# Optimization experiments

Measured on AMD Instinct MI355X. Metric: run time of the kernel, lower is better.

## Reference

```python
import jax, jax.numpy as jnp
import numpy as np

N = 50000      # nodes
E = 400000     # edges (before self-loops)
IN = 128       # in_channels
OUT = 64       # out_channels (per-head; concat=False averages heads)
HEADS = 8      # heads of first GAT layer; second layer has 1 head
NEG_SLOPE = 0.2


def _glorot(key, shape, fan_in, fan_out):
    s = jnp.sqrt(2.0 / (fan_in + fan_out)).astype(jnp.float32)
    return jax.random.normal(key, shape, jnp.float32) * s


def setup_inputs() -> dict:
    key = jax.random.key(0)
    ks = jax.random.split(key, 10)
    x = jax.random.normal(ks[0], (N, IN), jnp.float32)
    edge_index = jax.random.randint(ks[1], (2, E), 0, N)
    # layer 1: heads=HEADS, per-head dim OUT
    W1 = _glorot(ks[2], (IN, HEADS * OUT), IN, HEADS * OUT)
    att_src1 = _glorot(ks[3], (HEADS, OUT), OUT, 1)
    att_dst1 = _glorot(ks[4], (HEADS, OUT), OUT, 1)
    b1 = jnp.zeros((OUT,), jnp.float32)
    # layer 2: heads=1
    W2 = _glorot(ks[5], (OUT, 1 * OUT), OUT, OUT)
    att_src2 = _glorot(ks[6], (1, OUT), OUT, 1)
    att_dst2 = _glorot(ks[7], (1, OUT), OUT, 1)
    b2 = jnp.zeros((OUT,), jnp.float32)
    return dict(x=x, edge_index=edge_index, W1=W1, att_src1=att_src1,
                att_dst1=att_dst1, b1=b1, W2=W2, att_src2=att_src2,
                att_dst2=att_dst2, b2=b2)


def gat_conv(x, edge_index, W, att_src, att_dst, bias, heads, ch):
    """PyG GATConv with concat=False (mean over heads), add_self_loops=True."""
    n = x.shape[0]
    loop = jnp.arange(n, dtype=edge_index.dtype)
    src = jnp.concatenate([edge_index[0], loop])  # [E+N]
    dst = jnp.concatenate([edge_index[1], loop])
    h = (x @ W).reshape(n, heads, ch)                     # [N, H, C]
    a_s = jnp.sum(h * att_src, axis=-1)                   # [N, H]
    a_d = jnp.sum(h * att_dst, axis=-1)                   # [N, H]
    e = jax.nn.leaky_relu(a_s[src] + a_d[dst], NEG_SLOPE)  # [E+N, H]
    # numerically stable segment softmax over incoming edges of each dst node
    emax = jax.lax.stop_gradient(
        jax.ops.segment_max(e, dst, num_segments=n))       # [N, H]
    ee = jnp.exp(e - emax[dst])
    denom = jax.ops.segment_sum(ee, dst, num_segments=n)  # [N, H]
    alpha = ee / denom[dst]                                # [E+N, H]
    out = jax.ops.segment_sum(alpha[:, :, None] * h[src], dst,
                              num_segments=n)              # [N, H, C]
    return out.mean(axis=1) + bias                         # [N, C]


def reference(x, edge_index, W1, att_src1, att_dst1, b1,
              W2, att_src2, att_dst2, b2):
    h = gat_conv(x, edge_index, W1, att_src1, att_dst1, b1, HEADS, OUT)
    h = jax.nn.elu(h)
    return gat_conv(h, edge_index, W2, att_src2, att_dst2, b2, 1, OUT)
```

## Files before the change

kernel.cpp:

```cpp
#include <hip/hip_runtime.h>
#include <cstdint>
#include <cstddef>

#define NEG_SLOPE 0.2f

typedef short bf16x8 __attribute__((ext_vector_type(8)));
typedef float f32x4 __attribute__((ext_vector_type(4)));
typedef float f32x2 __attribute__((ext_vector_type(2)));

__device__ __forceinline__ unsigned short f2bf(float f) {
  unsigned u = __float_as_uint(f);
  u = u + 0x7FFFu + ((u >> 16) & 1u);
  return (unsigned short)(u >> 16);
}
__device__ __forceinline__ float bf2f(unsigned short b) {
  return __uint_as_float((unsigned)b << 16);
}
__device__ __forceinline__ f32x2 unpk(unsigned xv) {
  f32x2 r;
  r.x = __uint_as_float(xv << 16);
  r.y = __uint_as_float(xv & 0xFFFF0000u);
  return r;
}

__global__ __launch_bounds__(256) void prep_all(
    const int* __restrict__ ei, int* __restrict__ counts,
    const float* __restrict__ x, unsigned short* __restrict__ xb,
    const float* __restrict__ W1, const float* __restrict__ att_s1,
    const float* __restrict__ att_d1, unsigned short* __restrict__ AsAdT,
    unsigned short* __restrict__ WbT,
    const float* __restrict__ W2, unsigned short* __restrict__ W2t,
    const float* __restrict__ att_s2, const float* __restrict__ att_d2,
    float* __restrict__ AsAd2,
    int E, int ET, int N, int B0, int B1) {
  int b = blockIdx.x, tid = threadIdx.x;
  if (b < B0) {
    int i = b * 256 + tid;
    if (i < ET) {
      int dst = (i < E) ? ei[E + i] : (i - E);
      atomicAdd(&counts[dst], 1);
    }
    return;
  }
  b -= B0;
  if (b < B1) {
    int i = b * 256 + tid;
    if (i < N * 32) {
      float4 v = ((const float4*)x)[i];
      ushort4 o;
      o.x = f2bf(v.x); o.y = f2bf(v.y); o.z = f2bf(v.z); o.w = f2bf(v.w);
      ((ushort4*)xb)[i] = o;
    }
    return;
  }
  b -= B1;
  if (b < 8) {
    int i = b * 256 + tid;
    int o = i >> 7, k = i & 127, h = o & 7;
    const float* att = (o < 8) ? att_s1 : att_d1;
    float s = 0.f;
    for (int c = 0; c < 64; c++) s += W1[(size_t)k * 512 + h * 64 + c] * att[h * 64 + c];
    AsAdT[i] = f2bf(s);
    return;
  }
  b -= 8;
  if (b < 256) {
    int i = b * 256 + tid;
    int o = i >> 10, k = i & 1023, h = k >> 7, c = k & 127;
    WbT[i] = f2bf(W1[(size_t)c * 512 + h * 64 + o]);
    return;
  }
  b -= 256;
  if (b < 16) {
    int i = b * 256 + tid;
    if (i < 64 * 64) {
      int k = i >> 6, nn = i & 63;
      W2t[(size_t)nn * 64 + k] = f2bf(W2[i]);
    }
    return;
  }
  {
    int i = tid;
    if (i < 128) {
      int o = i >> 6, k = i & 63;
      const float* att = (o == 0) ? att_s2 : att_d2;
      float s = 0.f;
      for (int c = 0; c < 64; c++) s += W2[(size_t)k * 64 + c] * att[c];
      AsAd2[i] = s;
    }
  }
}

__global__ __launch_bounds__(1024) void scan_dots(
    const int* __restrict__ counts, int* __restrict__ offsets,
    const unsigned short* __restrict__ xb, const unsigned short* __restrict__ AsAdT,
    float* __restrict__ asd, int n) {
  if (blockIdx.x == 0) {
    __shared__ int sums[1024];
    int t = threadIdx.x;
    int chunk = (n + 1023) >> 10;
    int start = t * chunk;
    int end = min(start + chunk, n);
    int s = 0;
    for (int i = start; i < end; i++) s += counts[i];
    sums[t] = s;
    __syncthreads();
    for (int off = 1; off < 1024; off <<= 1) {
      int v = (t >= off) ? sums[t - off] : 0;
      __syncthreads();
      sums[t] += v;
      __syncthreads();
    }
    int run = sums[t] - s;
    for (int i = start; i < end; i++) { offsets[i] = run; run += counts[i]; }
    if (t == 1023) offsets[n] = sums[1023];
    return;
  }
  int tid = threadIdx.x;
  int wave = tid >> 6, lane = tid & 63;
  int q = lane >> 4, t = lane & 15;
  int row0 = (blockIdx.x - 1) * 256 + wave * 16;
  int arow = row0 + t; if (arow > n - 1) arow = n - 1;
  const bf16x8* aptr = (const bf16x8*)(xb + (size_t)arow * 128);
  const bf16x8* bptr = (const bf16x8*)(AsAdT + t * 128);
  f32x4 acc = (f32x4){0.f, 0.f, 0.f, 0.f};
  #pragma unroll
  for (int s = 0; s < 4; s++)
    acc = __builtin_amdgcn_mfma_f32_16x16x32_bf16(aptr[s * 4 + q], bptr[s * 4 + q],
                                                  acc, 0, 0, 0);
  #pragma unroll
  for (int r = 0; r < 4; r++) {
    int row = row0 + q * 4 + r;
    if (row < n) asd[row * 16 + t] = acc[r];
  }
}

__global__ __launch_bounds__(256) void fill_weights(
    const int* __restrict__ ei, const int* __restrict__ offsets,
    int* __restrict__ cursor, int* __restrict__ srcs,
    const float* __restrict__ asd, float* __restrict__ wbuf,
    int E, int ET) {
  int i = blockIdx.x * 256 + threadIdx.x;
  if (i >= ET) return;
  int src, dst;
  if (i < E) { src = ei[i]; dst = ei[E + i]; } else { src = dst = i - E; }
  int pos = atomicAdd(&cursor[dst], 1);
  int slot = offsets[dst] + pos;
  srcs[slot] = src;
  float4 s0 = *(const float4*)&asd[src * 16];
  float4 s1 = *(const float4*)&asd[src * 16 + 4];
  float4 d0 = *(const float4*)&asd[dst * 16 + 8];
  float4 d1 = *(const float4*)&asd[dst * 16 + 12];
  float w[8];
  w[0] = s0.x + d0.x; w[1] = s0.y + d0.y; w[2] = s0.z + d0.z; w[3] = s0.w + d0.w;
  w[4] = s1.x + d1.x; w[5] = s1.y + d1.y; w[6] = s1.z + d1.z; w[7] = s1.w + d1.w;
  #pragma unroll
  for (int h = 0; h < 8; h++) {
    float v = w[h];
    v = (v > 0.f) ? v : NEG_SLOPE * v;
    w[h] = __expf(v);
  }
  float4* wp = (float4*)&wbuf[(size_t)slot * 8];
  wp[0] = make_float4(w[0], w[1], w[2], w[3]);
  wp[1] = make_float4(w[4], w[5], w[6], w[7]);
}

__global__ __launch_bounds__(1024, 8) void agg1_gemm(
    const int* __restrict__ offsets, const int* __restrict__ srcs,
    const float* __restrict__ wbuf, const unsigned short* __restrict__ xb,
    const unsigned short* __restrict__ WbT, const float* __restrict__ b1,
    const float* __restrict__ AsAd2, unsigned short* __restrict__ zb,
    float* __restrict__ as2, float* __restrict__ ad2, int N) {
  __shared__ unsigned short sh[16 * 1032];
  __shared__ int ssrc[16][64];
  __shared__ float sas[16], sad[16];
  int tid = threadIdx.x;
  int wv = tid >> 6, lane = tid & 63;
  int nb = blockIdx.x;
  {
    int row = wv;
    int node = nb * 16 + row;
    float2 acc[8];
    float ws[8];
    #pragma unroll
    for (int h = 0; h < 8; h++) { acc[h].x = 0.f; acc[h].y = 0.f; ws[h] = 0.f; }
    int beg = offsets[node], end = offsets[node + 1];
    for (int cb = beg; cb < end; cb += 64) {
      int cnt = min(64, end - cb);
      if (lane < cnt) ssrc[row][lane] = srcs[cb + lane];
      #pragma unroll 4
      for (int k = 0; k < cnt; k++) {
        int s = ssrc[row][k];
        unsigned xv = *(const unsigned*)&xb[(size_t)s * 128 + 2 * lane];
        float4 wa = *(const float4*)&wbuf[(size_t)(cb + k) * 8];
        float4 wb = *(const float4*)&wbuf[(size_t)(cb + k) * 8 + 4];
        float x0 = __uint_as_float(xv << 16);
        float x1 = __uint_as_float(xv & 0xFFFF0000u);
        acc[0].x += wa.x * x0; acc[0].y += wa.x * x1; ws[0] += wa.x;
        acc[1].x += wa.y * x0; acc[1].y += wa.y * x1; ws[1] += wa.y;
        acc[2].x += wa.z * x0; acc[2].y += wa.z * x1; ws[2] += wa.z;
        acc[3].x += wa.w * x0; acc[3].y += wa.w * x1; ws[3] += wa.w;
        acc[4].x += wb.x * x0; acc[4].y += wb.x * x1; ws[4] += wb.x;
        acc[5].x += wb.y * x0; acc[5].y += wb.y * x1; ws[5] += wb.y;
        acc[6].x += wb.z * x0; acc[6].y += wb.z * x1; ws[6] += wb.z;
        acc[7].x += wb.w * x0; acc[7].y += wb.w * x1; ws[7] += wb.w;
      }
    }
    #pragma unroll
    for (int h = 0; h < 8; h++) {
      float iv = 0.125f / ws[h];
      unsigned o = (unsigned)f2bf(acc[h].x * iv) | ((unsigned)f2bf(acc[h].y * iv) << 16);
      *(unsigned*)&sh[row * 1032 + h * 128 + 2 * lane] = o;
    }
  }
  if (tid < 16) sas[tid] = 0.f;
  else if (tid < 32) sad[tid - 16] = 0.f;
  __syncthreads();
  if (wv < 4) {
    int q = lane >> 4, t = lane & 15;
    f32x4 acc4 = (f32x4){0.f, 0.f, 0.f, 0.f};
    const unsigned short* bbase = WbT + (size_t)(wv * 16 + t) * 1024;
    #pragma unroll 8
    for (int s = 0; s < 32; s++) {
      bf16x8 af = *(const bf16x8*)&sh[t * 1032 + s * 32 + q * 8];
      bf16x8 bf = *(const bf16x8*)&bbase[s * 32 + q * 8];
      acc4 = __builtin_amdgcn_mfma_f32_16x16x32_bf16(af, bf, acc4, 0, 0, 0);
    }
    int col = wv * 16 + t;
    float bias = b1[col];
    float vs = AsAd2[col], vd = AsAd2[64 + col];
    float zr[4];
    #pragma unroll
    for (int r = 0; r < 4; r++) {
      int row = q * 4 + r;
      int node = nb * 16 + row;
      float v = acc4[r] + bias;
      v = (v > 0.f) ? v : (__expf(v) - 1.f);
      zr[r] = v;
      zb[(size_t)node * 64 + col] = f2bf(v);
    }
    #pragma unroll
    for (int r = 0; r < 4; r++) {
      float s = zr[r] * vs, d = zr[r] * vd;
      #pragma unroll
      for (int off = 1; off < 16; off <<= 1) {
        s += __shfl_xor(s, off, 64);
        d += __shfl_xor(d, off, 64);
      }
      if (t == 0) {
        atomicAdd(&sas[q * 4 + r], s);
        atomicAdd(&sad[q * 4 + r], d);
      }
    }
  }
  __syncthreads();
  if (tid < 16) as2[nb * 16 + tid] = sas[tid];
  else if (tid < 32) ad2[nb * 16 + (tid - 16)] = sad[tid - 16];
}

__global__ __launch_bounds__(1024, 8) void agg2_gemm(
    const int* __restrict__ offsets, const int* __restrict__ srcs,
    const float* __restrict__ as2, const float* __restrict__ ad2,
    const unsigned short* __restrict__ zb, const unsigned short* __restrict__ W2t,
    const float* __restrict__ b2, float* __restrict__ out, int N) {
  __shared__ unsigned short sh[16 * 72];
  __shared__ int ssrc[16][64];
  int tid = threadIdx.x;
  int wv = tid >> 6, lane = tid & 63;
  int nb = blockIdx.x;
  {
    int row = wv;
    int node = nb * 16 + row;
    int half = lane >> 5;
    int l2 = lane & 31;
    float adv = ad2[node];
    int beg = offsets[node], end = offsets[node + 1];
    f32x2 acc = (f32x2){0.f, 0.f};
    float ws = 0.f;
    for (int cb = beg; cb < end; cb += 64) {
      int cnt = min(64, end - cb);
      if (lane < cnt) ssrc[row][lane] = srcs[cb + lane];
      #pragma unroll 2
      for (int k = half; k < cnt; k += 2) {
        int s = ssrc[row][k];
        float asv = as2[s];
        unsigned zv = *(const unsigned*)&zb[(size_t)s * 64 + 2 * l2];
        float v = asv + adv;
        v = (v > 0.f) ? v : NEG_SLOPE * v;
        float w = __expf(v);
        ws += w;
        acc += unpk(zv) * w;
      }
    }
    acc.x += __shfl_xor(acc.x, 32, 64);
    acc.y += __shfl_xor(acc.y, 32, 64);
    ws += __shfl_xor(ws, 32, 64);
    if (half == 0) {
      float inv = 1.f / ws;
      unsigned o = (unsigned)f2bf(acc.x * inv) | ((unsigned)f2bf(acc.y * inv) << 16);
      *(unsigned*)&sh[row * 72 + 2 * l2] = o;
    }
  }
  __syncthreads();
  if (wv < 4) {
    int q = lane >> 4, t = lane & 15;
    f32x4 acc4 = (f32x4){0.f, 0.f, 0.f, 0.f};
    const unsigned short* bbase = W2t + (size_t)(wv * 16 + t) * 64;
    #pragma unroll
    for (int s = 0; s < 2; s++) {
      bf16x8 af = *(const bf16x8*)&sh[t * 72 + s * 32 + q * 8];
      bf16x8 bf = *(const bf16x8*)&bbase[s * 32 + q * 8];
      acc4 = __builtin_amdgcn_mfma_f32_16x16x32_bf16(af, bf, acc4, 0, 0, 0);
    }
    int col = wv * 16 + t;
    float bias = b2[col];
    #pragma unroll
    for (int r = 0; r < 4; r++) {
      int node = nb * 16 + q * 4 + r;
      if (node < N) out[(size_t)node * 64 + col] = acc4[r] + bias;
    }
  }
}

extern "C" void kernel_launch(void* const* d_in, const int* in_sizes, int n_in,
                              void* d_out, int out_size, void* d_ws, size_t ws_size,
                              hipStream_t stream) {
  const int IN = 128;
  const int N = in_sizes[0] / IN;
  const int E = in_sizes[1] / 2;
  const int ET = E + N;

  const float* x        = (const float*)d_in[0];
  const int*   ei       = (const int*)d_in[1];
  const float* W1       = (const float*)d_in[2];
  const float* att_src1 = (const float*)d_in[3];
  const float* att_dst1 = (const float*)d_in[4];
  const float* b1       = (const float*)d_in[5];
  const float* W2       = (const float*)d_in[6];
  const float* att_src2 = (const float*)d_in[7];
  const float* att_dst2 = (const float*)d_in[8];
  const float* b2       = (const float*)d_in[9];
  float* out = (float*)d_out;

  char* base = (char*)d_ws;
  size_t off = 0;
  auto alloc = [&](size_t bytes) -> char* {
    char* p = base + off;
    off = (off + bytes + 255) & ~(size_t)255;
    return p;
  };
  unsigned short* xb    = (unsigned short*)alloc((size_t)N * 128 * 2);
  unsigned short* AsAdT = (unsigned short*)alloc((size_t)16 * 128 * 2);
  unsigned short* WbT   = (unsigned short*)alloc((size_t)64 * 1024 * 2);
  unsigned short* W2t   = (unsigned short*)alloc((size_t)64 * 64 * 2);
  unsigned short* zb    = (unsigned short*)alloc((size_t)N * 64 * 2);
  float* AsAd2 = (float*)alloc((size_t)128 * 4);
  float* asd1  = (float*)alloc((size_t)N * 16 * 4);
  float* a_s2  = (float*)alloc((size_t)N * 4);
  float* a_d2  = (float*)alloc((size_t)N * 4);
  float* wbuf  = (float*)alloc((size_t)ET * 8 * 4);
  int* offsets = (int*)alloc((size_t)(N + 1) * 4);
  int* srcs    = (int*)alloc((size_t)ET * 4);
  char* zero_begin = base + off;
  int* counts  = (int*)alloc((size_t)N * 4);
  int* cursor  = (int*)alloc((size_t)N * 4);
  char* zero_end = base + off;

  hipMemsetAsync(zero_begin, 0, (size_t)(zero_end - zero_begin), stream);

  const int TB = 256;
  auto cdiv = [](int a, int b) { return (a + b - 1) / b; };

  int B0 = cdiv(ET, TB);
  int B1 = cdiv(N * 32, TB);
  prep_all<<<B0 + B1 + 8 + 256 + 16 + 1, TB, 0, stream>>>(
      ei, counts, x, xb, W1, att_src1, att_dst1, AsAdT, WbT, W2, W2t,
      att_src2, att_dst2, AsAd2, E, ET, N, B0, B1);

  scan_dots<<<1 + cdiv(N, 256), 1024, 0, stream>>>(counts, offsets, xb, AsAdT,
                                                   asd1, N);

  fill_weights<<<cdiv(ET, TB), TB, 0, stream>>>(ei, offsets, cursor, srcs,
                                                asd1, wbuf, E, ET);

  agg1_gemm<<<cdiv(N, 16), 1024, 0, stream>>>(offsets, srcs, wbuf, xb, WbT, b1,
                                              AsAd2, zb, a_s2, a_d2, N);

  agg2_gemm<<<cdiv(N, 16), 1024, 0, stream>>>(offsets, srcs, a_s2, a_d2, zb,
                                              W2t, b2, out, N);
}
```

Measured before the change: 355.8 us.

## Stage neighbor feature rows into LDS via async global_load_lds with prefetched indices

The per-node gather loop in agg1_gemm now fetches 8 source rows per iteration straight into LDS with global_load_lds DMA. It prefetches the next chunk's source indices and attention weights into registers while the current chunk is consumed, and broadcasts weights with lane shuffles instead of per-edge float4 loads. The goal is to overlap the irregular gather latency with the FMA work and to cut redundant wbuf loads. The risks are shuffle overhead, a waitcnt that stalls on all loads, and reuse of the sh staging buffer that the later GEMM also uses.

```diff
diff --git a/kernel.cpp b/kernel.cpp
--- a/kernel.cpp
+++ b/kernel.cpp
@@ -21,6 +21,11 @@
   r.x = __uint_as_float(xv << 16);
   r.y = __uint_as_float(xv & 0xFFFF0000u);
   return r;
+}
+__device__ __forceinline__ void dma16(const unsigned short* g, unsigned short* l) {
+  __builtin_amdgcn_global_load_lds(
+      (const __attribute__((address_space(1))) unsigned*)g,
+      (__attribute__((address_space(3))) unsigned*)l, 16, 0, 0);
 }
 
 __global__ __launch_bounds__(256) void prep_all(
@@ -172,7 +177,6 @@
     const float* __restrict__ AsAd2, unsigned short* __restrict__ zb,
     float* __restrict__ as2, float* __restrict__ ad2, int N) {
   __shared__ unsigned short sh[16 * 1032];
-  __shared__ int ssrc[16][64];
   __shared__ float sas[16], sad[16];
   int tid = threadIdx.x;
   int wv = tid >> 6, lane = tid & 63;
@@ -180,30 +184,50 @@
   {
     int row = wv;
     int node = nb * 16 + row;
-    float2 acc[8];
+    unsigned short* stg = &sh[row * 1032];
+    f32x2 acc[8];
     float ws[8];
     #pragma unroll
-    for (int h = 0; h < 8; h++) { acc[h].x = 0.f; acc[h].y = 0.f; ws[h] = 0.f; }
+    for (int h = 0; h < 8; h++) { acc[h] = (f32x2){0.f, 0.f}; ws[h] = 0.f; }
     int beg = offsets[node], end = offsets[node + 1];
-    for (int cb = beg; cb < end; cb += 64) {
-      int cnt = min(64, end - cb);
-      if (lane < cnt) ssrc[row][lane] = srcs[cb + lane];
-      #pragma unroll 4
+    int jl = end - 1;
+    int e0 = min(beg + (lane >> 4), jl);
+    int e1 = min(beg + 4 + (lane >> 4), jl);
+    int s0 = srcs[e0], s1 = srcs[e1];
+    int we = min(beg + (lane >> 3), jl);
+    float wl = wbuf[(size_t)we * 8 + (lane & 7)];
+    for (int cb = beg; cb < end; cb += 8) {
+      dma16(xb + (size_t)s0 * 128 + (lane & 15) * 8, stg);
+      dma16(xb + (size_t)s1 * 128 + (lane & 15) * 8, stg + 512);
+      float wcur = wl;
+      int cn = cb + 8;
+      int e0n = min(cn + (lane >> 4), jl);
+      int e1n = min(cn + 4 + (lane >> 4), jl);
+      s0 = srcs[e0n];
+      s1 = srcs[e1n];
+      int wen = min(cn + (lane >> 3), jl);
+      wl = wbuf[(size_t)wen * 8 + (lane & 7)];
+      __builtin_amdgcn_s_waitcnt(0x0f70);
+      int cnt = min(8, end - cb);
       for (int k = 0; k < cnt; k++) {
-        int s = ssrc[row][k];
-        unsigned xv = *(const unsigned*)&xb[(size_t)s * 128 + 2 * lane];
-        float4 wa = *(const float4*)&wbuf[(size_t)(cb + k) * 8];
-        float4 wb = *(const float4*)&wbuf[(size_t)(cb + k) * 8 + 4];
-        float x0 = __uint_as_float(xv << 16);
-        float x1 = __uint_as_float(xv & 0xFFFF0000u);
-        acc[0].x += wa.x * x0; acc[0].y += wa.x * x1; ws[0] += wa.x;
-        acc[1].x += wa.y * x0; acc[1].y += wa.y * x1; ws[1] += wa.y;
-        acc[2].x += wa.z * x0; acc[2].y += wa.z * x1; ws[2] += wa.z;
-        acc[3].x += wa.w * x0; acc[3].y += wa.w * x1; ws[3] += wa.w;
-        acc[4].x += wb.x * x0; acc[4].y += wb.x * x1; ws[4] += wb.x;
-        acc[5].x += wb.y * x0; acc[5].y += wb.y * x1; ws[5] += wb.y;
-        acc[6].x += wb.z * x0; acc[6].y += wb.z * x1; ws[6] += wb.z;
-        acc[7].x += wb.w * x0; acc[7].y += wb.w * x1; ws[7] += wb.w;
+        float w0 = __shfl(wcur, k * 8 + 0, 64);
+        float w1 = __shfl(wcur, k * 8 + 1, 64);
+        float w2 = __shfl(wcur, k * 8 + 2, 64);
+        float w3 = __shfl(wcur, k * 8 + 3, 64);
+        float w4 = __shfl(wcur, k * 8 + 4, 64);
+        float w5 = __shfl(wcur, k * 8 + 5, 64);
+        float w6 = __shfl(wcur, k * 8 + 6, 64);
+        float w7 = __shfl(wcur, k * 8 + 7, 64);
+        unsigned xv = *(const unsigned*)&stg[k * 128 + 2 * lane];
+        f32x2 x2 = unpk(xv);
+        acc[0] += x2 * w0; ws[0] += w0;
+        acc[1] += x2 * w1; ws[1] += w1;
+        acc[2] += x2 * w2; ws[2] += w2;
+        acc[3] += x2 * w3; ws[3] += w3;
+        acc[4] += x2 * w4; ws[4] += w4;
+        acc[5] += x2 * w5; ws[5] += w5;
+        acc[6] += x2 * w6; ws[6] += w6;
+        acc[7] += x2 * w7; ws[7] += w7;
       }
     }
     #pragma unroll
```

Result: faster. 338.1 us (-5.0%).
